# Performance work log

Measured on AMD Instinct MI355X. Metric: run time of the kernel, lower is better.

## Reference

```python
import jax, jax.numpy as jnp
import numpy as np

B, S, D, H, K = 2, 2048, 1024, 16, 16


def setup_inputs() -> dict:
    key = jax.random.key(0)
    ks = jax.random.split(key, 8)
    s = 0.02
    def w(k, shape):
        return s * jax.random.normal(k, shape, jnp.float32)
    return {
        "x": jax.random.normal(ks[0], (B, S, D), jnp.float32),
        "Wq": w(ks[1], (D, D)), "bq": jnp.zeros((D,), jnp.float32),
        "Wk": w(ks[2], (D, D)), "bk": jnp.zeros((D,), jnp.float32),
        "Wv": w(ks[3], (D, D)), "bv": jnp.zeros((D,), jnp.float32),
        "Wo": w(ks[4], (D, D)), "bo": jnp.zeros((D,), jnp.float32),
        "Ws1": w(ks[5], (D, D // 2)), "bs1": jnp.zeros((D // 2,), jnp.float32),
        "Ws2": w(ks[6], (D // 2, 1)), "bs2": jnp.zeros((1,), jnp.float32),
    }


def reference(x, Wq, bq, Wk, bk, Wv, bv, Wo, bo, Ws1, bs1, Ws2, bs2):
    Bx, Sx, Dx = x.shape
    Dh = Dx // H
    # QKV projections -> [B, H, S, Dh]
    q = (x @ Wq + bq).reshape(Bx, Sx, H, Dh).transpose(0, 2, 1, 3)
    k = (x @ Wk + bk).reshape(Bx, Sx, H, Dh).transpose(0, 2, 1, 3)
    v = (x @ Wv + bv).reshape(Bx, Sx, H, Dh).transpose(0, 2, 1, 3)
    scores = jnp.einsum('bhqd,bhkd->bhqk', q, k) / np.float32(np.sqrt(Dh))
    # Lightning-indexer importance: [B, S]; identical across heads, so compute once.
    imp = jax.nn.sigmoid(jax.nn.relu(x @ Ws1 + bs1) @ Ws2 + bs2)[..., 0]
    _, idx = jax.lax.top_k(imp, K)  # [B, K]
    sel = jnp.zeros((Bx, Sx), bool).at[jnp.arange(Bx)[:, None], idx].set(True)
    # sparse mask: position (i, j) kept if row i OR column j is a top-k token
    m2 = sel[:, :, None] | sel[:, None, :]  # [B, S, S]
    masked = jnp.where(m2[:, None, :, :], scores, -jnp.inf)
    w = jax.nn.softmax(masked, axis=-1)
    att = jnp.einsum('bhqk,bhkd->bhqd', w, v).transpose(0, 2, 1, 3).reshape(Bx, Sx, Dx)
    return att @ Wo + bo
```

## Files before the change

### kernel.cpp

```cpp
#include <hip/hip_runtime.h>
#include <math.h>

constexpr int Bb = 2, Ss = 2048, Dd = 1024, Hh = 16, Kk = 16;
constexpr float DELTA = 0.02f;

typedef __bf16 bf16x8 __attribute__((ext_vector_type(8)));
typedef __bf16 bf16x4 __attribute__((ext_vector_type(4)));
typedef float  f32x4  __attribute__((ext_vector_type(4)));

__device__ __forceinline__ void gld_lds16(const void* g, void* l) {
    __builtin_amdgcn_global_load_lds(
        (const __attribute__((address_space(1))) unsigned int*)g,
        (__attribute__((address_space(3))) unsigned int*)l, 16, 0, 0);
}

__global__ void __launch_bounds__(512) gemm_qkv_ind(
    const __bf16* __restrict__ xb, const __bf16* __restrict__ WqkvT,
    const __bf16* __restrict__ W1Th,
    const float* __restrict__ bq, const float* __restrict__ bk,
    const float* __restrict__ bv,
    __bf16* __restrict__ qb, __bf16* __restrict__ kb, __bf16* __restrict__ vb,
    const float* __restrict__ bs1, const float* __restrict__ Ws2,
    float* __restrict__ imp)
{
    __shared__ __bf16 As[256 * 64];
    __shared__ __bf16 Bs[128 * 64];

    const int bid  = blockIdx.x;
    const int cb   = bid % 28;
    const int bm   = (bid / 28) * 256;
    const int t    = threadIdx.x;
    const int wave = t >> 6;
    const int lane = t & 63;
    const int fr   = lane & 15;
    const int fq   = lane >> 4;
    const int K    = Dd;
    const bool ind = (cb >= 24);

    const __bf16* BT = ind ? (W1Th + (size_t)(cb - 24) * 128 * 1024)
                           : (WqkvT + (size_t)cb * 128 * 1024);

    const int wm = (wave & 3) * 64;
    const int wn = (wave >> 2) * 64;

    f32x4 acc[4][4] = {};

    for (int k0 = 0; k0 < K; k0 += 64) {
        #pragma unroll
        for (int l = 0; l < 4; ++l) {
            int c = l * 512 + t;
            int row = c >> 3, seg = (c & 7) ^ (row & 7);
            gld_lds16(xb + (size_t)(bm + row) * K + k0 + seg * 8,
                      As + (size_t)(l * 512 + wave * 64) * 8);
        }
        #pragma unroll
        for (int l = 0; l < 2; ++l) {
            int c = l * 512 + t;
            int row = c >> 3, seg = (c & 7) ^ (row & 7);
            gld_lds16(BT + (size_t)row * K + k0 + seg * 8,
                      Bs + (size_t)(l * 512 + wave * 64) * 8);
        }
        __syncthreads();

        #pragma unroll
        for (int s = 0; s < 2; ++s) {
            bf16x8 af[4], bf[4];
            #pragma unroll
            for (int i = 0; i < 4; ++i) {
                int row = wm + i * 16 + fr;
                af[i] = *(const bf16x8*)(As + row * 64 + (((s * 4 + fq) ^ (row & 7)) * 8));
            }
            #pragma unroll
            for (int j = 0; j < 4; ++j) {
                int row = wn + j * 16 + fr;
                bf[j] = *(const bf16x8*)(Bs + row * 64 + (((s * 4 + fq) ^ (row & 7)) * 8));
            }
            #pragma unroll
            for (int i = 0; i < 4; ++i)
                #pragma unroll
                for (int j = 0; j < 4; ++j)
                    acc[i][j] = __builtin_amdgcn_mfma_f32_16x16x32_bf16(af[i], bf[j], acc[i][j], 0, 0, 0);
        }
        __syncthreads();
    }

    const int cr = (lane >> 4) * 4;
    const int cc = lane & 15;

    if (!ind) {
        const int zone = cb >> 3;
        const int cl0  = cb * 128 - zone * 1024;
        const float* bias = (zone == 0) ? bq : (zone == 1) ? bk : bv;
        __bf16*      C    = (zone == 0) ? qb : (zone == 1) ? kb : vb;
        #pragma unroll
        for (int j = 0; j < 4; ++j) {
            int col = cl0 + wn + j * 16 + cc;
            float bb = bias[col];
            #pragma unroll
            for (int i = 0; i < 4; ++i) {
                #pragma unroll
                for (int r = 0; r < 4; ++r)
                    C[(size_t)(bm + wm + i * 16 + cr + r) * Dd + col] =
                        (__bf16)(acc[i][j][r] + bb);
            }
        }
    } else {
        const int hc0 = (cb - 24) * 128;
        float bb[4], w2[4];
        #pragma unroll
        for (int j = 0; j < 4; ++j) {
            int col = hc0 + wn + j * 16 + cc;
            bb[j] = bs1[col];
            w2[j] = Ws2[col];
        }
        #pragma unroll
        for (int i = 0; i < 4; ++i) {
            #pragma unroll
            for (int r = 0; r < 4; ++r) {
                float vsum = 0.f;
                #pragma unroll
                for (int j = 0; j < 4; ++j)
                    vsum += fmaxf(acc[i][j][r] + bb[j], 0.f) * w2[j];
                #pragma unroll
                for (int off = 8; off > 0; off >>= 1)
                    vsum += __shfl_xor(vsum, off, 16);
                if (cc == 0)
                    atomicAdd(imp + (bm + wm + i * 16 + cr + r), vsum);
            }
        }
    }
}

__global__ void __launch_bounds__(256) gemm_out(
    const __bf16* __restrict__ A, const __bf16* __restrict__ BT,
    const float* __restrict__ bias, float* __restrict__ C, int M, int N, int K)
{
    __shared__ __bf16 As[64 * 64];
    __shared__ __bf16 Bs[128 * 64];

    const int t    = threadIdx.x;
    const int wave = t >> 6;
    const int lane = t & 63;
    const int bm   = blockIdx.y * 64;
    const int bn   = blockIdx.x * 128;
    const int wm   = (wave & 1) * 32;
    const int wn   = (wave >> 1) * 64;
    const int fr   = lane & 15;
    const int fq   = lane >> 4;

    f32x4 acc[2][4] = {};

    for (int k0 = 0; k0 < K; k0 += 64) {
        #pragma unroll
        for (int l = 0; l < 2; ++l) {
            int c = l * 256 + t;
            int row = c >> 3, seg = (c & 7) ^ (row & 7);
            gld_lds16(A + (size_t)(bm + row) * K + k0 + seg * 8,
                      As + (size_t)(l * 256 + wave * 64) * 8);
        }
        #pragma unroll
        for (int l = 0; l < 4; ++l) {
            int c = l * 256 + t;
            int row = c >> 3, seg = (c & 7) ^ (row & 7);
            gld_lds16(BT + (size_t)(bn + row) * K + k0 + seg * 8,
                      Bs + (size_t)(l * 256 + wave * 64) * 8);
        }
        __syncthreads();

        #pragma unroll
        for (int s = 0; s < 2; ++s) {
            bf16x8 af[2], bf[4];
            #pragma unroll
            for (int i = 0; i < 2; ++i) {
                int row = wm + i * 16 + fr;
                af[i] = *(const bf16x8*)(As + row * 64 + (((s * 4 + fq) ^ (row & 7)) * 8));
            }
            #pragma unroll
            for (int j = 0; j < 4; ++j) {
                int row = wn + j * 16 + fr;
                bf[j] = *(const bf16x8*)(Bs + row * 64 + (((s * 4 + fq) ^ (row & 7)) * 8));
            }
            #pragma unroll
            for (int i = 0; i < 2; ++i)
                #pragma unroll
                for (int j = 0; j < 4; ++j)
                    acc[i][j] = __builtin_amdgcn_mfma_f32_16x16x32_bf16(af[i], bf[j], acc[i][j], 0, 0, 0);
        }
        __syncthreads();
    }

    const int cr = (lane >> 4) * 4;
    const int cc = lane & 15;
    #pragma unroll
    for (int j = 0; j < 4; ++j) {
        int col = bn + wn + j * 16 + cc;
        float bb = bias[col];
        #pragma unroll
        for (int i = 0; i < 2; ++i) {
            #pragma unroll
            for (int r = 0; r < 4; ++r)
                C[(size_t)(bm + wm + i * 16 + cr + r) * N + col] = acc[i][j][r] + bb;
        }
    }
}

__global__ void __launch_bounds__(256) prep_kernel(
    const float* __restrict__ x, __bf16* __restrict__ xb,
    float* __restrict__ imp, float* __restrict__ oacc,
    float* __restrict__ lsum, float* __restrict__ hbuf,
    int* __restrict__ ccount,
    const float* __restrict__ W0, const float* __restrict__ W1,
    const float* __restrict__ W2, const float* __restrict__ W3,
    __bf16* __restrict__ WqkvT, __bf16* __restrict__ WoT,
    const float* __restrict__ Ws1, __bf16* __restrict__ Th)
{
    __shared__ float tile[32][33];
    const int bid = blockIdx.x;

    if (bid < 4096) {
        int i = bid * 256 + threadIdx.x;
        if (i < Bb * Ss) imp[i] = 0.f;
        if (i < Bb * Hh * Kk * 64) oacc[i] = 0.f;
        if (i < Bb * Hh * Kk) lsum[i] = 0.f;
        if (i < Bb * 64 * 512) hbuf[i] = 0.f;
        if (i < Bb) ccount[i] = 0;
        float4 v = ((const float4*)x)[i];
        bf16x4 h = { (__bf16)v.x, (__bf16)v.y, (__bf16)v.z, (__bf16)v.w };
        ((bf16x4*)xb)[i] = h;
        return;
    }

    int tid = bid - 4096;
    int z   = tid >> 10;
    int rem = tid & 1023;
    int n0  = (rem & 31) * 32;
    int k0  = (rem >> 5) * 32;
    int tx = threadIdx.x & 31, ty = threadIdx.x >> 5;

    if (z < 4) {
        const float* W = (z == 0) ? W0 : (z == 1) ? W1 : (z == 2) ? W2 : W3;
        __bf16*      T = (z < 3) ? (WqkvT + (size_t)z * 1024 * 1024) : WoT;
        #pragma unroll
        for (int i = 0; i < 32; i += 8)
            tile[ty + i][tx] = W[(size_t)(k0 + ty + i) * 1024 + n0 + tx];
        __syncthreads();
        #pragma unroll
        for (int i = 0; i < 32; i += 8)
            T[(size_t)(n0 + ty + i) * 1024 + k0 + tx] = (__bf16)tile[tx][ty + i];
    } else {
        if (n0 >= 512) return;
        #pragma unroll
        for (int i = 0; i < 32; i += 8)
            tile[ty + i][tx] = Ws1[(size_t)(k0 + ty + i) * 512 + n0 + tx];
        __syncthreads();
        #pragma unroll
        for (int i = 0; i < 32; i += 8)
            Th[(size_t)(n0 + ty + i) * 1024 + k0 + tx] = (__bf16)tile[tx][ty + i];
    }
}

__global__ void __launch_bounds__(1024) topk_cand(
    const float* __restrict__ imp, int* __restrict__ cand_idx,
    int* __restrict__ ccount)
{
    int b = blockIdx.x;
    int t = threadIdx.x;
    int wave = t >> 6, lane = t & 63;
    __shared__ float vals[Ss];
    __shared__ float sv[16];
    __shared__ int   si[16];
    __shared__ float thr_s;
    __shared__ int   cnt_s;

    vals[t]        = imp[b * Ss + t];
    vals[t + 1024] = imp[b * Ss + t + 1024];
    __syncthreads();

    for (int it = 0; it < Kk; ++it) {
        float v0 = vals[t], v1 = vals[t + 1024];
        float best = v0; int bidx = t;
        if (v1 > best) { best = v1; bidx = t + 1024; }
        #pragma unroll
        for (int off = 32; off > 0; off >>= 1) {
            float ov = __shfl_xor(best, off, 64);
            int   oi = __shfl_xor(bidx, off, 64);
            if (ov > best || (ov == best && oi < bidx)) { best = ov; bidx = oi; }
        }
        if (lane == 0) { sv[wave] = best; si[wave] = bidx; }
        __syncthreads();
        if (t == 0) {
            float bv = sv[0]; int br = si[0];
            #pragma unroll
            for (int w = 1; w < 16; ++w)
                if (sv[w] > bv || (sv[w] == bv && si[w] < br)) { bv = sv[w]; br = si[w]; }
            cand_idx[b * 64 + it] = br;
            vals[br] = -1e30f;
            if (it == Kk - 1) { thr_s = bv - DELTA; cnt_s = Kk; }
        }
        __syncthreads();
    }

    float thr = thr_s;
    if (vals[t] > thr) {
        int p = atomicAdd(&cnt_s, 1);
        if (p < 64) cand_idx[b * 64 + p] = t;
    }
    if (vals[t + 1024] > thr) {
        int p = atomicAdd(&cnt_s, 1);
        if (p < 64) cand_idx[b * 64 + p] = t + 1024;
    }
    __syncthreads();
    if (t == 0) ccount[b] = min(cnt_s, 64);
}

__global__ void __launch_bounds__(256) rescore_h(
    const float* __restrict__ x, const float* __restrict__ Ws1,
    const int* __restrict__ cand_idx, const int* __restrict__ ccount,
    float* __restrict__ hbuf)
{
    const int c = blockIdx.x, kc = blockIdx.y, b = blockIdx.z;
    if (c >= ccount[b]) return;
    const int row = cand_idx[b * 64 + c];
    const int t = threadIdx.x;
    const int k0 = kc * 64;

    __shared__ float xs[64];
    if (t < 16)
        ((float4*)xs)[t] = ((const float4*)(x + ((size_t)(b * Ss + row)) * Dd + k0))[t];
    __syncthreads();

    float a0 = 0.f, a1 = 0.f;
    const float* W = Ws1 + (size_t)k0 * 512;
    #pragma unroll 16
    for (int kk = 0; kk < 64; ++kk) {
        float xv = xs[kk];
        a0 = fmaf(xv, W[kk * 512 + t], a0);
        a1 = fmaf(xv, W[kk * 512 + t + 256], a1);
    }
    float* hb = hbuf + ((size_t)(b * 64 + c)) * 512;
    atomicAdd(hb + t, a0);
    atomicAdd(hb + t + 256, a1);
}

__global__ void __launch_bounds__(256) rescore_fin(
    const float* __restrict__ hbuf, const float* __restrict__ bs1,
    const float* __restrict__ Ws2, const int* __restrict__ ccount,
    float* __restrict__ candz)
{
    const int c = blockIdx.x, b = blockIdx.y;
    if (c >= ccount[b]) return;
    const int t = threadIdx.x;
    __shared__ float red[256];
    const float* hb = hbuf + ((size_t)(b * 64 + c)) * 512;
    float zp = fmaxf(hb[t] + bs1[t], 0.f) * Ws2[t]
             + fmaxf(hb[t + 256] + bs1[t + 256], 0.f) * Ws2[t + 256];
    red[t] = zp;
    __syncthreads();
    for (int off = 128; off > 0; off >>= 1) {
        if (t < off) red[t] += red[t + off];
        __syncthreads();
    }
    if (t == 0) candz[b * 64 + c] = red[0];
}

__global__ void __launch_bounds__(64) select_k(
    const float* __restrict__ candz, const int* __restrict__ cand_idx,
    const int* __restrict__ ccount, int* __restrict__ sel_idx)
{
    const int b = blockIdx.x, t = threadIdx.x;
    const int cnt = ccount[b];
    float val = (t < cnt) ? candz[b * 64 + t] : -1e30f;
    int   row = (t < cnt) ? cand_idx[b * 64 + t] : 0x7fffffff;

    for (int it = 0; it < Kk; ++it) {
        float bv = val; int br = row;
        #pragma unroll
        for (int off = 1; off < 64; off <<= 1) {
            float ov = __shfl_xor(bv, off, 64);
            int   orw = __shfl_xor(br, off, 64);
            if (ov > bv || (ov == bv && orw < br)) { bv = ov; br = orw; }
        }
        if (row == br) val = -1e30f;
        if (t == 0) sel_idx[b * Kk + it] = br;
    }
}

__global__ void __launch_bounds__(256) attn_all(
    const __bf16* __restrict__ q, const __bf16* __restrict__ k,
    const __bf16* __restrict__ v, const int* __restrict__ sel_idx,
    __bf16* __restrict__ att, float* __restrict__ lsum,
    float* __restrict__ oacc)
{
    __shared__ __align__(16) float sm[6720];
    const int b = blockIdx.z, h = blockIdx.y;
    const int t = threadIdx.x;

    if (blockIdx.x < 128) {
        float (*KT)[17]  = (float(*)[17])sm;
        float (*Vs)[64]  = (float(*)[64])(sm + 1088);
        float (*qsh)[65] = (float(*)[65])(sm + 2112);
        float (*wsh)[16] = (float(*)[16])(sm + 3152);
        int*  sj         = (int*)(sm + 3408);
        const int q0 = blockIdx.x * 16;

        if (t < 16) sj[t] = sel_idx[b * Kk + t];
        __syncthreads();

        {
            int row = t >> 4, d0 = (t & 15) * 4;
            bf16x4 kv = *(const bf16x4*)(k + ((size_t)(b * Ss + sj[row])) * Dd + h * 64 + d0);
            bf16x4 vv = *(const bf16x4*)(v + ((size_t)(b * Ss + sj[row])) * Dd + h * 64 + d0);
            bf16x4 qv = *(const bf16x4*)(q + ((size_t)(b * Ss + q0 + row)) * Dd + h * 64 + d0);
            #pragma unroll
            for (int i = 0; i < 4; ++i) {
                KT[d0 + i][row]  = (float)kv[i];
                Vs[row][d0 + i]  = (float)vv[i];
                qsh[row][d0 + i] = (float)qv[i];
            }
        }
        __syncthreads();

        const int wave = t >> 6, lane = t & 63;
        const int ql = lane >> 4, j = lane & 15;
        const int qi = wave * 4 + ql;

        float s = 0.f;
        #pragma unroll
        for (int d = 0; d < 64; ++d) s = fmaf(qsh[qi][d], KT[d][j], s);
        s *= 0.125f;

        float m = s;
        #pragma unroll
        for (int off = 8; off > 0; off >>= 1) m = fmaxf(m, __shfl_xor(m, off, 16));
        float e = __expf(s - m);
        float sum = e;
        #pragma unroll
        for (int off = 8; off > 0; off >>= 1) sum += __shfl_xor(sum, off, 16);
        wsh[qi][j] = e / sum;

        #pragma unroll
        for (int q2 = 0; q2 < 4; ++q2) {
            int qq = wave * 4 + q2;
            float o = 0.f;
            #pragma unroll
            for (int jj = 0; jj < 16; ++jj)
                o = fmaf(wsh[qq][jj], Vs[jj][lane], o);
            att[((size_t)(b * Ss + q0 + qq)) * Dd + h * 64 + lane] = (__bf16)o;
        }
    } else {
        float (*Ks)[68] = (float(*)[68])sm;
        float (*Qs)[68] = (float(*)[68])(sm + 4352);
        float (*Es)[80] = (float(*)[80])(sm + 5440);
        const int j0 = (blockIdx.x - 128) * 64;

        #pragma unroll
        for (int l = 0; l < 2; ++l) {
            int c = t + 256 * l;
            int row = c >> 3, seg = c & 7;
            bf16x8 kv = *(const bf16x8*)(k + ((size_t)(b * Ss + j0 + row)) * Dd + h * 64 + seg * 8);
            #pragma unroll
            for (int e = 0; e < 8; ++e) Ks[row][seg * 8 + e] = (float)kv[e];
        }
        if (t < 128) {
            int row = t >> 3, seg = t & 7;
            int i = sel_idx[b * Kk + row];
            bf16x8 qv = *(const bf16x8*)(q + ((size_t)(b * Ss + i)) * Dd + h * 64 + seg * 8);
            #pragma unroll
            for (int e = 0; e < 8; ++e) Qs[row][seg * 8 + e] = (float)qv[e];
        }
        __syncthreads();

        const int qi = t >> 4, ks = t & 15;
        const int bhq = (b * Hh + h) * Kk + qi;
        float psum = 0.f;
        #pragma unroll
        for (int s8 = 0; s8 < 4; ++s8) {
            int j = ks + s8 * 16;
            float sdot = 0.f;
            #pragma unroll
            for (int d4 = 0; d4 < 16; ++d4) {
                float4 qv = *(const float4*)&Qs[qi][d4 * 4];
                float4 kv = *(const float4*)&Ks[j][d4 * 4];
                sdot += qv.x * kv.x + qv.y * kv.y + qv.z * kv.z + qv.w * kv.w;
            }
            float e = __expf(sdot * 0.125f);
            Es[qi][j] = e;
            psum += e;
        }
        #pragma unroll
        for (int off = 8; off > 0; off >>= 1) psum += __shfl_xor(psum, off, 16);
        if (ks == 0) atomicAdd(lsum + bhq, psum);
        __syncthreads();

        #pragma unroll
        for (int l = 0; l < 2; ++l) {
            int c = t + 256 * l;
            int row = c >> 3, seg = c & 7;
            bf16x8 vv = *(const bf16x8*)(v + ((size_t)(b * Ss + j0 + row)) * Dd + h * 64 + seg * 8);
            #pragma unroll
            for (int e = 0; e < 8; ++e) Ks[row][seg * 8 + e] = (float)vv[e];
        }
        __syncthreads();

        const int d = t & 63, qg = t >> 6;
        #pragma unroll
        for (int qq = 0; qq < 4; ++qq) {
            int qx = qg * 4 + qq;
            float o = 0.f;
            #pragma unroll 8
            for (int jj = 0; jj < 64; ++jj)
                o = fmaf(Es[qx][jj], Ks[jj][d], o);
            atomicAdd(oacc + (size_t)((b * Hh + h) * Kk + qx) * 64 + d, o);
        }
    }
}

__global__ void __launch_bounds__(64) attn_dense_fin(
    const float* __restrict__ oacc, const float* __restrict__ lsum,
    const int* __restrict__ sel_idx, __bf16* __restrict__ att)
{
    int bid = blockIdx.x;
    int qi = bid & 15, h = (bid >> 4) & 15, b = bid >> 8;
    int bhq = (b * Hh + h) * Kk + qi;
    int i = sel_idx[b * Kk + qi];
    float val = oacc[(size_t)bhq * 64 + threadIdx.x] / lsum[bhq];
    att[((size_t)(b * Ss + i)) * Dd + h * 64 + threadIdx.x] = (__bf16)val;
}

extern "C" void kernel_launch(void* const* d_in, const int* in_sizes, int n_in,
                              void* d_out, int out_size, void* d_ws, size_t ws_size,
                              hipStream_t stream)
{
    const float* x   = (const float*)d_in[0];
    const float* Wq  = (const float*)d_in[1];
    const float* bq  = (const float*)d_in[2];
    const float* Wk  = (const float*)d_in[3];
    const float* bk  = (const float*)d_in[4];
    const float* Wv  = (const float*)d_in[5];
    const float* bv  = (const float*)d_in[6];
    const float* Wo  = (const float*)d_in[7];
    const float* bo  = (const float*)d_in[8];
    const float* Ws1 = (const float*)d_in[9];
    const float* bs1 = (const float*)d_in[10];
    const float* Ws2 = (const float*)d_in[11];
    float* out = (float*)d_out;

    const size_t MSD = (size_t)Bb * Ss * Dd;
    const int M = Bb * Ss;

    char* p = (char*)d_ws;
    __bf16* qb  = (__bf16*)p; p += MSD * sizeof(__bf16);
    __bf16* kb  = (__bf16*)p; p += MSD * sizeof(__bf16);
    __bf16* vb  = (__bf16*)p; p += MSD * sizeof(__bf16);
    __bf16* att = (__bf16*)p; p += MSD * sizeof(__bf16);
    __bf16* xb  = (__bf16*)p; p += MSD * sizeof(__bf16);
    __bf16* WqkvT = (__bf16*)p; p += (size_t)3 * Dd * Dd * sizeof(__bf16);
    __bf16* WoT   = (__bf16*)p; p += (size_t)Dd * Dd * sizeof(__bf16);
    __bf16* W1Th  = (__bf16*)p; p += (size_t)512 * Dd * sizeof(__bf16);
    float* imp  = (float*)p; p += (size_t)Bb * Ss * sizeof(float);
    int* sel_idx = (int*)p; p += (size_t)Bb * Kk * sizeof(int);
    float* oacc = (float*)p; p += (size_t)Bb * Hh * Kk * 64 * sizeof(float);
    float* lsum = (float*)p; p += (size_t)Bb * Hh * Kk * sizeof(float);
    float* hbuf = (float*)p; p += (size_t)Bb * 64 * 512 * sizeof(float);
    int* ccount   = (int*)p; p += Bb * sizeof(int);
    int* cand_idx = (int*)p; p += (size_t)Bb * 64 * sizeof(int);
    float* candz  = (float*)p; p += (size_t)Bb * 64 * sizeof(float);

    prep_kernel<<<dim3(4096 + 5120), 256, 0, stream>>>(
        x, xb, imp, oacc, lsum, hbuf, ccount,
        Wq, Wk, Wv, Wo, WqkvT, WoT, Ws1, W1Th);
    gemm_qkv_ind<<<dim3(448), 512, 0, stream>>>(
        xb, WqkvT, W1Th, bq, bk, bv, qb, kb, vb, bs1, Ws2, imp);
    topk_cand<<<dim3(Bb), 1024, 0, stream>>>(imp, cand_idx, ccount);
    rescore_h<<<dim3(64, 16, Bb), 256, 0, stream>>>(x, Ws1, cand_idx, ccount, hbuf);
    rescore_fin<<<dim3(64, Bb), 256, 0, stream>>>(hbuf, bs1, Ws2, ccount, candz);
    select_k<<<dim3(Bb), 64, 0, stream>>>(candz, cand_idx, ccount, sel_idx);
    attn_all<<<dim3(160, Hh, Bb), 256, 0, stream>>>(
        qb, kb, vb, sel_idx, att, lsum, oacc);
    attn_dense_fin<<<dim3(Bb * Hh * Kk), 64, 0, stream>>>(oacc, lsum, sel_idx, att);
    gemm_out<<<dim3(8, 64), 256, 0, stream>>>(att, WoT, bo, out, M, Dd, Dd);
}
```

Before: 240.4 us.

## Restructure sparse attention algebraically to avoid full QKV projections and output GEMM

Replaces the full Q/K/V projection GEMM and full output projection with an algebraic reformulation. It projects only the selected top-k tokens' Q/K/V, folds Wq·k_sel and Wk·q_sel into small effective weight matrices (ET), and computes scores directly from x. Values are folded through Wo (VoT), so non-selected rows become a small x-by-256 GEMM and selected rows are handled by separate dense kernels. This removes most of the large bf16 projection work at the cost of many new kernels, a transposed copy of x, and different rounding paths.

Result: slower. 399.4 us (+66.2%).

```diff
diff --git a/kernel.cpp b/kernel.cpp
--- a/kernel.cpp
+++ b/kernel.cpp
@@ -14,12 +14,63 @@
         (__attribute__((address_space(3))) unsigned int*)l, 16, 0, 0);
 }
 
-__global__ void __launch_bounds__(512) gemm_qkv_ind(
-    const __bf16* __restrict__ xb, const __bf16* __restrict__ WqkvT,
-    const __bf16* __restrict__ W1Th,
-    const float* __restrict__ bq, const float* __restrict__ bk,
-    const float* __restrict__ bv,
-    __bf16* __restrict__ qb, __bf16* __restrict__ kb, __bf16* __restrict__ vb,
+__global__ void __launch_bounds__(256) prep_kernel(
+    const float* __restrict__ x, __bf16* __restrict__ xb,
+    __bf16* __restrict__ xbT,
+    float* __restrict__ imp, float* __restrict__ hbuf,
+    float* __restrict__ qkvsel, int* __restrict__ ccount,
+    const float* __restrict__ Ws1, __bf16* __restrict__ W1Th)
+{
+    __shared__ float tile[32][33];
+    const int bid = blockIdx.x;
+    const int t   = threadIdx.x;
+
+    if (bid < 4096) {
+        int i = bid * 256 + t;
+        if (i < Bb * Ss) imp[i] = 0.f;
+        if (i < Bb * 64 * 512) hbuf[i] = 0.f;
+        if (i < 3 * 32 * 1024) qkvsel[i] = 0.f;
+        if (i < Bb) ccount[i] = 0;
+        float4 v = ((const float4*)x)[i];
+        bf16x4 h = { (__bf16)v.x, (__bf16)v.y, (__bf16)v.z, (__bf16)v.w };
+        ((bf16x4*)xb)[i] = h;
+        return;
+    }
+    if (bid < 8192) {
+        int tid = bid - 4096;
+        int b   = tid >> 11;
+        int rem = tid & 2047;
+        int rt  = rem >> 5;
+        int ct  = rem & 31;
+        int tx = t & 31, ty = t >> 5;
+        const float* xp = x + (size_t)b * Ss * Dd;
+        #pragma unroll
+        for (int i2 = 0; i2 < 32; i2 += 8)
+            tile[ty + i2][tx] = xp[(size_t)(rt * 32 + ty + i2) * 1024 + ct * 32 + tx];
+        __syncthreads();
+        __bf16* xT = xbT + (size_t)b * Dd * Ss;
+        #pragma unroll
+        for (int i2 = 0; i2 < 32; i2 += 8)
+            xT[(size_t)(ct * 32 + ty + i2) * 2048 + rt * 32 + tx] = (__bf16)tile[tx][ty + i2];
+        return;
+    }
+    {
+        int tid = bid - 8192;
+        int n0 = (tid & 15) * 32;
+        int k0 = (tid >> 4) * 32;
+        int tx = t & 31, ty = t >> 5;
+        #pragma unroll
+        for (int i2 = 0; i2 < 32; i2 += 8)
+            tile[ty + i2][tx] = Ws1[(size_t)(k0 + ty + i2) * 512 + n0 + tx];
+        __syncthreads();
+        #pragma unroll
+        for (int i2 = 0; i2 < 32; i2 += 8)
+            W1Th[(size_t)(n0 + ty + i2) * 1024 + k0 + tx] = (__bf16)tile[tx][ty + i2];
+    }
+}
+
+__global__ void __launch_bounds__(512) gemm_ind(
+    const __bf16* __restrict__ xb, const __bf16* __restrict__ W1Th,
     const float* __restrict__ bs1, const float* __restrict__ Ws2,
     float* __restrict__ imp)
 {
@@ -27,19 +78,16 @@
     __shared__ __bf16 Bs[128 * 64];
 
     const int bid  = blockIdx.x;
-    const int cb   = bid % 28;
-    const int bm   = (bid / 28) * 256;
+    const int cb   = bid & 3;
+    const int bm   = (bid >> 2) * 256;
     const int t    = threadIdx.x;
     const int wave = t >> 6;
     const int lane = t & 63;
     const int fr   = lane & 15;
     const int fq   = lane >> 4;
     const int K    = Dd;
-    const bool ind = (cb >= 24);
-
-    const __bf16* BT = ind ? (W1Th + (size_t)(cb - 24) * 128 * 1024)
-                           : (WqkvT + (size_t)cb * 128 * 1024);
-
+
+    const __bf16* BT = W1Th + (size_t)cb * 128 * 1024;
     const int wm = (wave & 3) * 64;
     const int wn = (wave >> 2) * 64;
 
@@ -61,7 +109,6 @@
                       Bs + (size_t)(l * 512 + wave * 64) * 8);
         }
         __syncthreads();
-
         #pragma unroll
         for (int s = 0; s < 2; ++s) {
             bf16x8 af[4], bf[4];
@@ -86,57 +133,446 @@
 
     const int cr = (lane >> 4) * 4;
     const int cc = lane & 15;
-
-    if (!ind) {
-        const int zone = cb >> 3;
-        const int cl0  = cb * 128 - zone * 1024;
-        const float* bias = (zone == 0) ? bq : (zone == 1) ? bk : bv;
-        __bf16*      C    = (zone == 0) ? qb : (zone == 1) ? kb : vb;
-        #pragma unroll
-        for (int j = 0; j < 4; ++j) {
-            int col = cl0 + wn + j * 16 + cc;
-            float bb = bias[col];
+    const int hc0 = cb * 128;
+    float bb[4], w2[4];
+    #pragma unroll
+    for (int j = 0; j < 4; ++j) {
+        int col = hc0 + wn + j * 16 + cc;
+        bb[j] = bs1[col];
+        w2[j] = Ws2[col];
+    }
+    #pragma unroll
+    for (int i = 0; i < 4; ++i) {
+        #pragma unroll
+        for (int r = 0; r < 4; ++r) {
+            float vsum = 0.f;
+            #pragma unroll
+            for (int j = 0; j < 4; ++j)
+                vsum += fmaxf(acc[i][j][r] + bb[j], 0.f) * w2[j];
+            #pragma unroll
+            for (int off = 8; off > 0; off >>= 1)
+                vsum += __shfl_xor(vsum, off, 16);
+            if (cc == 0)
+                atomicAdd(imp + (bm + wm + i * 16 + cr + r), vsum);
+        }
+    }
+}
+
+__global__ void __launch_bounds__(1024) topk_cand(
+    const float* __restrict__ imp, int* __restrict__ cand_idx,
+    int* __restrict__ ccount)
+{
+    int b = blockIdx.x;
+    int t = threadIdx.x;
+    int wave = t >> 6, lane = t & 63;
+    __shared__ float vals[Ss];
+    __shared__ float sv[16];
+    __shared__ int   si[16];
+    __shared__ float thr_s;
+    __shared__ int   cnt_s;
+
+    vals[t]        = imp[b * Ss + t];
+    vals[t + 1024] = imp[b * Ss + t + 1024];
+    __syncthreads();
+
+    for (int it = 0; it < Kk; ++it) {
+        float v0 = vals[t], v1 = vals[t + 1024];
+        float best = v0; int bidx = t;
+        if (v1 > best) { best = v1; bidx = t + 1024; }
+        #pragma unroll
+        for (int off = 32; off > 0; off >>= 1) {
+            float ov = __shfl_xor(best, off, 64);
+            int   oi = __shfl_xor(bidx, off, 64);
+            if (ov > best || (ov == best && oi < bidx)) { best = ov; bidx = oi; }
+        }
+        if (lane == 0) { sv[wave] = best; si[wave] = bidx; }
+        __syncthreads();
+        if (t == 0) {
+            float bv = sv[0]; int br = si[0];
+            #pragma unroll
+            for (int w = 1; w < 16; ++w)
+                if (sv[w] > bv || (sv[w] == bv && si[w] < br)) { bv = sv[w]; br = si[w]; }
+            cand_idx[b * 64 + it] = br;
+            vals[br] = -1e30f;
+            if (it == Kk - 1) { thr_s = bv - DELTA; cnt_s = Kk; }
+        }
+        __syncthreads();
+    }
+
+    float thr = thr_s;
+    if (vals[t] > thr) {
+        int p = atomicAdd(&cnt_s, 1);
+        if (p < 64) cand_idx[b * 64 + p] = t;
+    }
+    if (vals[t + 1024] > thr) {
+        int p = atomicAdd(&cnt_s, 1);
+        if (p < 64) cand_idx[b * 64 + p] = t + 1024;
+    }
+    __syncthreads();
+    if (t == 0) ccount[b] = min(cnt_s, 64);
+}
+
+__global__ void __launch_bounds__(256) rescore_h(
+    const float* __restrict__ x, const float* __restrict__ Ws1,
+    const int* __restrict__ cand_idx, const int* __restrict__ ccount,
+    float* __restrict__ hbuf)
+{
+    const int c = blockIdx.x, kc = blockIdx.y, b = blockIdx.z;
+    if (c >= ccount[b]) return;
+    const int row = cand_idx[b * 64 + c];
+    const int t = threadIdx.x;
+    const int k0 = kc * 64;
+
+    __shared__ float xs[64];
+    if (t < 16)
+        ((float4*)xs)[t] = ((const float4*)(x + ((size_t)(b * Ss + row)) * Dd + k0))[t];
+    __syncthreads();
+
+    float a0 = 0.f, a1 = 0.f;
+    const float* W = Ws1 + (size_t)k0 * 512;
+    #pragma unroll 16
+    for (int kk = 0; kk < 64; ++kk) {
+        float xv = xs[kk];
+        a0 = fmaf(xv, W[kk * 512 + t], a0);
+        a1 = fmaf(xv, W[kk * 512 + t + 256], a1);
+    }
+    float* hb = hbuf + ((size_t)(b * 64 + c)) * 512;
+    atomicAdd(hb + t, a0);
+    atomicAdd(hb + t + 256, a1);
+}
+
+__global__ void __launch_bounds__(256) rescore_fin(
+    const float* __restrict__ hbuf, const float* __restrict__ bs1,
+    const float* __restrict__ Ws2, const int* __restrict__ ccount,
+    float* __restrict__ candz)
+{
+    const int c = blockIdx.x, b = blockIdx.y;
+    if (c >= ccount[b]) return;
+    const int t = threadIdx.x;
+    __shared__ float red[256];
+    const float* hb = hbuf + ((size_t)(b * 64 + c)) * 512;
+    float zp = fmaxf(hb[t] + bs1[t], 0.f) * Ws2[t]
+             + fmaxf(hb[t + 256] + bs1[t + 256], 0.f) * Ws2[t + 256];
+    red[t] = zp;
+    __syncthreads();
+    for (int off = 128; off > 0; off >>= 1) {
+        if (t < off) red[t] += red[t + off];
+        __syncthreads();
+    }
+    if (t == 0) candz[b * 64 + c] = red[0];
+}
+
+__global__ void __launch_bounds__(64) select_k(
+    const float* __restrict__ candz, const int* __restrict__ cand_idx,
+    const int* __restrict__ ccount, int* __restrict__ sel_idx)
+{
+    const int b = blockIdx.x, t = threadIdx.x;
+    const int cnt = ccount[b];
+    float val = (t < cnt) ? candz[b * 64 + t] : -1e30f;
+    int   row = (t < cnt) ? cand_idx[b * 64 + t] : 0x7fffffff;
+
+    for (int it = 0; it < Kk; ++it) {
+        float bv = val; int br = row;
+        #pragma unroll
+        for (int off = 1; off < 64; off <<= 1) {
+            float ov = __shfl_xor(bv, off, 64);
+            int   orw = __shfl_xor(br, off, 64);
+            if (ov > bv || (ov == bv && orw < br)) { bv = ov; br = orw; }
+        }
+        if (row == br) val = -1e30f;
+        if (t == 0) sel_idx[b * Kk + it] = br;
+    }
+}
+
+__global__ void __launch_bounds__(256) proj_sel(
+    const float* __restrict__ x,
+    const float* __restrict__ Wq, const float* __restrict__ Wk,
+    const float* __restrict__ Wv,
+    const int* __restrict__ sel_idx, float* __restrict__ qkvsel)
+{
+    const int cx = blockIdx.x;
+    const int m  = blockIdx.y;
+    const int kc = blockIdx.z;
+    const int t  = threadIdx.x;
+    __shared__ int   sj[32];
+    __shared__ float xs[32][128];
+
+    if (t < 32) sj[t] = sel_idx[t];
+    __syncthreads();
+
+    const int k0 = kc * 128;
+    #pragma unroll
+    for (int l = 0; l < 4; ++l) {
+        int c = l * 256 + t;
+        int r = c >> 5, kq = c & 31;
+        int b = r >> 4;
+        float4 v = *(const float4*)(x + ((size_t)(b * Ss + sj[r])) * Dd + k0 + kq * 4);
+        *(float4*)&xs[r][kq * 4] = v;
+    }
+    __syncthreads();
+
+    const float* W = (m == 0) ? Wq : (m == 1) ? Wk : Wv;
+    const int col = cx * 128 + (t & 127);
+    const int rh  = t >> 7;
+    float acc[16] = {};
+    #pragma unroll 4
+    for (int kk = 0; kk < 128; ++kk) {
+        float wv = W[(size_t)(k0 + kk) * 1024 + col];
+        #pragma unroll
+        for (int r = 0; r < 16; ++r)
+            acc[r] = fmaf(xs[rh * 16 + r][kk], wv, acc[r]);
+    }
+    #pragma unroll
+    for (int r = 0; r < 16; ++r)
+        atomicAdd(qkvsel + (size_t)(m * 32 + rh * 16 + r) * 1024 + col, acc[r]);
+}
+
+__global__ void __launch_bounds__(256) build_cdvo(
+    const float* __restrict__ Wq, const float* __restrict__ Wk,
+    const float* __restrict__ Wo,
+    const float* __restrict__ bq, const float* __restrict__ bk,
+    const float* __restrict__ bv,
+    const float* __restrict__ qkvsel, float* __restrict__ beta,
+    __bf16* __restrict__ ET, __bf16* __restrict__ VoT)
+{
+    const int nx = blockIdx.x;
+    const int h  = blockIdx.y;
+    const int b  = blockIdx.z;
+    const int t  = threadIdx.x;
+    __shared__ float qs[16][64], ks[16][64], vs[16][64];
+    __shared__ float wt[128][65];
+
+    #pragma unroll
+    for (int l = 0; l < 12; ++l) {
+        int c = l * 256 + t;
+        int mat = c >> 10, rem = c & 1023;
+        int row = rem >> 6, d = rem & 63;
+        const float* bias = (mat == 0) ? bq : (mat == 1) ? bk : bv;
+        float v = qkvsel[(size_t)(mat * 32 + b * 16 + row) * 1024 + h * 64 + d]
+                + bias[h * 64 + d];
+        if (mat == 0) qs[row][d] = v;
+        else if (mat == 1) ks[row][d] = v;
+        else vs[row][d] = v;
+    }
+    __syncthreads();
+
+    if (nx == 0 && t < 16) {
+        float a = 0.f;
+        #pragma unroll 8
+        for (int d = 0; d < 64; ++d) a = fmaf(bq[h * 64 + d], ks[t][d], a);
+        beta[b * 256 + h * 16 + t] = a;
+    }
+
+    const int nl = t & 127;
+    const int n  = nx * 128 + nl;
+    const int sg = t >> 7;
+
+    #pragma unroll
+    for (int l = 0; l < 8; ++l) {
+        int c = l * 256 + t;
+        int rn = c >> 4, c4 = c & 15;
+        float4 v = *(const float4*)(Wq + (size_t)(nx * 128 + rn) * 1024 + h * 64 + c4 * 4);
+        wt[rn][c4 * 4 + 0] = v.x; wt[rn][c4 * 4 + 1] = v.y;
+        wt[rn][c4 * 4 + 2] = v.z; wt[rn][c4 * 4 + 3] = v.w;
+    }
+    __syncthreads();
+    {
+        float acc[8] = {};
+        #pragma unroll 8
+        for (int d = 0; d < 64; ++d) {
+            float wv = wt[nl][d];
+            #pragma unroll
+            for (int s = 0; s < 8; ++s)
+                acc[s] = fmaf(wv, ks[sg * 8 + s][d], acc[s]);
+        }
+        #pragma unroll
+        for (int s = 0; s < 8; ++s)
+            ET[(size_t)(b * 512 + h * 16 + sg * 8 + s) * 1024 + n] = (__bf16)acc[s];
+    }
+    __syncthreads();
+
+    #pragma unroll
+    for (int l = 0; l < 8; ++l) {
+        int c = l * 256 + t;
+        int rn = c >> 4, c4 = c & 15;
+        float4 v = *(const float4*)(Wk + (size_t)(nx * 128 + rn) * 1024 + h * 64 + c4 * 4);
+        wt[rn][c4 * 4 + 0] = v.x; wt[rn][c4 * 4 + 1] = v.y;
+        wt[rn][c4 * 4 + 2] = v.z; wt[rn][c4 * 4 + 3] = v.w;
+    }
+    __syncthreads();
+    {
+        float acc[8] = {};
+        #pragma unroll 8
+        for (int d = 0; d < 64; ++d) {
+            float wv = wt[nl][d];
+            #pragma unroll
+            for (int s = 0; s < 8; ++s)
+                acc[s] = fmaf(wv, qs[sg * 8 + s][d], acc[s]);
+        }
+        #pragma unroll
+        for (int s = 0; s < 8; ++s)
+            ET[(size_t)(b * 512 + 256 + h * 16 + sg * 8 + s) * 1024 + n] = (__bf16)acc[s];
+    }
+
+    {
+        float acc[8] = {};
+        #pragma unroll 8
+        for (int d = 0; d < 64; ++d) {
+            float wv = Wo[(size_t)(h * 64 + d) * 1024 + n];
+            #pragma unroll
+            for (int s = 0; s < 8; ++s)
+                acc[s] = fmaf(wv, vs[sg * 8 + s][d], acc[s]);
+        }
+        #pragma unroll
+        for (int s = 0; s < 8; ++s)
+            VoT[((size_t)b * 1024 + n) * 256 + h * 16 + sg * 8 + s] = (__bf16)acc[s];
+    }
+}
+
+__global__ void __launch_bounds__(512) gemm_scores(
+    const __bf16* __restrict__ xb, const __bf16* __restrict__ ET,
+    float* __restrict__ Ssp, float* __restrict__ SdT)
+{
+    __shared__ __bf16 As[256 * 64];
+    __shared__ __bf16 Bs[128 * 64];
+
+    const int b    = blockIdx.y;
+    const int cb   = blockIdx.x & 3;
+    const int bm   = (blockIdx.x >> 2) * 256;
+    const int t    = threadIdx.x;
+    const int wave = t >> 6;
+    const int lane = t & 63;
+    const int fr   = lane & 15;
+    const int fq   = lane >> 4;
+    const int K    = Dd;
+
+    const __bf16* A  = xb + (size_t)b * Ss * Dd;
+    const __bf16* BT = ET + (size_t)b * 512 * 1024 + (size_t)cb * 128 * 1024;
+    const int wm = (wave & 3) * 64;
+    const int wn = (wave >> 2) * 64;
+
+    f32x4 acc[4][4] = {};
+
+    for (int k0 = 0; k0 < K; k0 += 64) {
+        #pragma unroll
+        for (int l = 0; l < 4; ++l) {
+            int c = l * 512 + t;
+            int row = c >> 3, seg = (c & 7) ^ (row & 7);
+            gld_lds16(A + (size_t)(bm + row) * K + k0 + seg * 8,
+                      As + (size_t)(l * 512 + wave * 64) * 8);
+        }
+        #pragma unroll
+        for (int l = 0; l < 2; ++l) {
+            int c = l * 512 + t;
+            int row = c >> 3, seg = (c & 7) ^ (row & 7);
+            gld_lds16(BT + (size_t)row * K + k0 + seg * 8,
+                      Bs + (size_t)(l * 512 + wave * 64) * 8);
+        }
+        __syncthreads();
+        #pragma unroll
+        for (int s = 0; s < 2; ++s) {
+            bf16x8 af[4], bf[4];
             #pragma unroll
             for (int i = 0; i < 4; ++i) {
+                int row = wm + i * 16 + fr;
+                af[i] = *(const bf16x8*)(As + row * 64 + (((s * 4 + fq) ^ (row & 7)) * 8));
+            }
+            #pragma unroll
+            for (int j = 0; j < 4; ++j) {
+                int row = wn + j * 16 + fr;
+                bf[j] = *(const bf16x8*)(Bs + row * 64 + (((s * 4 + fq) ^ (row & 7)) * 8));
+            }
+            #pragma unroll
+            for (int i = 0; i < 4; ++i)
+                #pragma unroll
+                for (int j = 0; j < 4; ++j)
+                    acc[i][j] = __builtin_amdgcn_mfma_f32_16x16x32_bf16(af[i], bf[j], acc[i][j], 0, 0, 0);
+        }
+        __syncthreads();
+    }
+
+    const int cr = (lane >> 4) * 4;
+    const int cc = lane & 15;
+    #pragma unroll
+    for (int j = 0; j < 4; ++j) {
+        int col = cb * 128 + wn + j * 16 + cc;
+        #pragma unroll
+        for (int i = 0; i < 4; ++i) {
+            int row0 = bm + wm + i * 16 + cr;
+            if (col < 256) {
                 #pragma unroll
                 for (int r = 0; r < 4; ++r)
-                    C[(size_t)(bm + wm + i * 16 + cr + r) * Dd + col] =
-                        (__bf16)(acc[i][j][r] + bb);
+                    Ssp[((size_t)b * 2048 + row0 + r) * 256 + col] = acc[i][j][r];
+            } else {
+                *(f32x4*)(SdT + ((size_t)b * 256 + col - 256) * 2048 + row0) = acc[i][j];
             }
         }
-    } else {
-        const int hc0 = (cb - 24) * 128;
-        float bb[4], w2[4];
-        #pragma unroll
-        for (int j = 0; j < 4; ++j) {
-            int col = hc0 + wn + j * 16 + cc;
-            bb[j] = bs1[col];
-            w2[j] = Ws2[col];
-        }
-        #pragma unroll
-        for (int i = 0; i < 4; ++i) {
-            #pragma unroll
-            for (int r = 0; r < 4; ++r) {
-                float vsum = 0.f;
-                #pragma unroll
-                for (int j = 0; j < 4; ++j)
-                    vsum += fmaxf(acc[i][j][r] + bb[j], 0.f) * w2[j];
-                #pragma unroll
-                for (int off = 8; off > 0; off >>= 1)
-                    vsum += __shfl_xor(vsum, off, 16);
-                if (cc == 0)
-                    atomicAdd(imp + (bm + wm + i * 16 + cr + r), vsum);
-            }
-        }
-    }
-}
-
-__global__ void __launch_bounds__(256) gemm_out(
-    const __bf16* __restrict__ A, const __bf16* __restrict__ BT,
-    const float* __restrict__ bias, float* __restrict__ C, int M, int N, int K)
+    }
+}
+
+__global__ void __launch_bounds__(256) sm_sparse(
+    const float* __restrict__ Ssp, const float* __restrict__ beta,
+    __bf16* __restrict__ Wsp)
+{
+    const int b = blockIdx.y;
+    const int r = blockIdx.x * 4 + (threadIdx.x >> 6);
+    const int l = threadIdx.x & 63;
+    float4 v  = *(const float4*)(Ssp + ((size_t)b * 2048 + r) * 256 + l * 4);
+    float4 bt = *(const float4*)(beta + b * 256 + l * 4);
+    float e0 = __expf((v.x + bt.x) * 0.125f);
+    float e1 = __expf((v.y + bt.y) * 0.125f);
+    float e2 = __expf((v.z + bt.z) * 0.125f);
+    float e3 = __expf((v.w + bt.w) * 0.125f);
+    float ps = e0 + e1 + e2 + e3;
+    ps += __shfl_xor(ps, 1, 64);
+    ps += __shfl_xor(ps, 2, 64);
+    float inv = 1.f / ps;
+    bf16x4 w = { (__bf16)(e0 * inv), (__bf16)(e1 * inv),
+                 (__bf16)(e2 * inv), (__bf16)(e3 * inv) };
+    *(bf16x4*)(Wsp + ((size_t)b * 2048 + r) * 256 + l * 4) = w;
+}
+
+__global__ void __launch_bounds__(256) sm_dense(
+    const float* __restrict__ SdT, __bf16* __restrict__ WdT)
+{
+    const int b = blockIdx.y, cx = blockIdx.x;
+    const int t = threadIdx.x;
+    __shared__ float red[256];
+    const float* Sp = SdT + ((size_t)b * 256 + cx) * 2048;
+    float4 v0 = *(const float4*)(Sp + t * 8);
+    float4 v1 = *(const float4*)(Sp + t * 8 + 4);
+    float e[8];
+    e[0] = __expf(v0.x * 0.125f); e[1] = __expf(v0.y * 0.125f);
+    e[2] = __expf(v0.z * 0.125f); e[3] = __expf(v0.w * 0.125f);
+    e[4] = __expf(v1.x * 0.125f); e[5] = __expf(v1.y * 0.125f);
+    e[6] = __expf(v1.z * 0.125f); e[7] = __expf(v1.w * 0.125f);
+    float ps = 0.f;
+    #pragma unroll
+    for (int i = 0; i < 8; ++i) ps += e[i];
+    red[t] = ps;
+    __syncthreads();
+    for (int off = 128; off > 0; off >>= 1) {
+        if (t < off) red[t] += red[t + off];
+        __syncthreads();
+    }
+    float inv = 1.f / red[0];
+    bf16x8 w;
+    #pragma unroll
+    for (int i = 0; i < 8; ++i) w[i] = (__bf16)(e[i] * inv);
+    *(bf16x8*)(WdT + ((size_t)b * 256 + cx) * 2048 + t * 8) = w;
+}
+
+__global__ void __launch_bounds__(256) gemm_bt(
+    const __bf16* __restrict__ A0, const __bf16* __restrict__ BT0,
+    const float* __restrict__ bias, float* __restrict__ C0,
+    int N, int K, size_t sA, size_t sB, size_t sC)
 {
     __shared__ __bf16 As[64 * 64];
     __shared__ __bf16 Bs[128 * 64];
+
+    const __bf16* A  = A0 + (size_t)blockIdx.z * sA;
+    const __bf16* BT = BT0 + (size_t)blockIdx.z * sB;
+    float* C = C0 + (size_t)blockIdx.z * sC;
 
     const int t    = threadIdx.x;
     const int wave = t >> 6;
@@ -166,7 +602,6 @@
                       Bs + (size_t)(l * 256 + wave * 64) * 8);
         }
         __syncthreads();
-
         #pragma unroll
         for (int s = 0; s < 2; ++s) {
             bf16x8 af[2], bf[4];
@@ -194,7 +629,7 @@
     #pragma unroll
     for (int j = 0; j < 4; ++j) {
         int col = bn + wn + j * 16 + cc;
-        float bb = bias[col];
+        float bb = bias ? bias[col] : 0.f;
         #pragma unroll
         for (int i = 0; i < 2; ++i) {
             #pragma unroll
@@ -204,327 +639,69 @@
     }
 }
 
-__global__ void __launch_bounds__(256) prep_kernel(
-    const float* __restrict__ x, __bf16* __restrict__ xb,
-    float* __restrict__ imp, float* __restrict__ oacc,
-    float* __restrict__ lsum, float* __restrict__ hbuf,
-    int* __restrict__ ccount,
-    const float* __restrict__ W0, const float* __restrict__ W1,
-    const float* __restrict__ W2, const float* __restrict__ W3,
-    __bf16* __restrict__ WqkvT, __bf16* __restrict__ WoT,
-    const float* __restrict__ Ws1, __bf16* __restrict__ Th)
-{
-    __shared__ float tile[32][33];
-    const int bid = blockIdx.x;
-
-    if (bid < 4096) {
-        int i = bid * 256 + threadIdx.x;
-        if (i < Bb * Ss) imp[i] = 0.f;
-        if (i < Bb * Hh * Kk * 64) oacc[i] = 0.f;
-        if (i < Bb * Hh * Kk) lsum[i] = 0.f;
-        if (i < Bb * 64 * 512) hbuf[i] = 0.f;
-        if (i < Bb) ccount[i] = 0;
-        float4 v = ((const float4*)x)[i];
-        bf16x4 h = { (__bf16)v.x, (__bf16)v.y, (__bf16)v.z, (__bf16)v.w };
-        ((bf16x4*)xb)[i] = h;
-        return;
-    }
-
-    int tid = bid - 4096;
-    int z   = tid >> 10;
-    int rem = tid & 1023;
-    int n0  = (rem & 31) * 32;
-    int k0  = (rem >> 5) * 32;
-    int tx = threadIdx.x & 31, ty = threadIdx.x >> 5;
-
-    if (z < 4) {
-        const float* W = (z == 0) ? W0 : (z == 1) ? W1 : (z == 2) ? W2 : W3;
-        __bf16*      T = (z < 3) ? (WqkvT + (size_t)z * 1024 * 1024) : WoT;
-        #pragma unroll
-        for (int i = 0; i < 32; i += 8)
-            tile[ty + i][tx] = W[(size_t)(k0 + ty + i) * 1024 + n0 + tx];
-        __syncthreads();
-        #pragma unroll
-        for (int i = 0; i < 32; i += 8)
-            T[(size_t)(n0 + ty + i) * 1024 + k0 + tx] = (__bf16)tile[tx][ty + i];
-    } else {
-        if (n0 >= 512) return;
-        #pragma unroll
-        for (int i = 0; i < 32; i += 8)
-            tile[ty + i][tx] = Ws1[(size_t)(k0 + ty + i) * 512 + n0 + tx];
-        __syncthreads();
-        #pragma unroll
-        for (int i = 0; i < 32; i += 8)
-            Th[(size_t)(n0 + ty + i) * 1024 + k0 + tx] = (__bf16)tile[tx][ty + i];
-    }
-}
-
-__global__ void __launch_bounds__(1024) topk_cand(
-    const float* __restrict__ imp, int* __restrict__ cand_idx,
-    int* __restrict__ ccount)
-{
-    int b = blockIdx.x;
-    int t = threadIdx.x;
-    int wave = t >> 6, lane = t & 63;
-    __shared__ float vals[Ss];
-    __shared__ float sv[16];
-    __shared__ int   si[16];
-    __shared__ float thr_s;
-    __shared__ int   cnt_s;
-
-    vals[t]        = imp[b * Ss + t];
-    vals[t + 1024] = imp[b * Ss + t + 1024];
-    __syncthreads();
-
-    for (int it = 0; it < Kk; ++it) {
-        float v0 = vals[t], v1 = vals[t + 1024];
-        float best = v0; int bidx = t;
-        if (v1 > best) { best = v1; bidx = t + 1024; }
-        #pragma unroll
-        for (int off = 32; off > 0; off >>= 1) {
-            float ov = __shfl_xor(best, off, 64);
-            int   oi = __shfl_xor(bidx, off, 64);
-            if (ov > best || (ov == best && oi < bidx)) { best = ov; bidx = oi; }
-        }
-        if (lane == 0) { sv[wave] = best; si[wave] = bidx; }
-        __syncthreads();
-        if (t == 0) {
-            float bv = sv[0]; int br = si[0];
-            #pragma unroll
-            for (int w = 1; w < 16; ++w)
-                if (sv[w] > bv || (sv[w] == bv && si[w] < br)) { bv = sv[w]; br = si[w]; }
-            cand_idx[b * 64 + it] = br;
-            vals[br] = -1e30f;
-            if (it == Kk - 1) { thr_s = bv - DELTA; cnt_s = Kk; }
-        }
-        __syncthreads();
-    }
-
-    float thr = thr_s;
-    if (vals[t] > thr) {
-        int p = atomicAdd(&cnt_s, 1);
-        if (p < 64) cand_idx[b * 64 + p] = t;
-    }
-    if (vals[t + 1024] > thr) {
-        int p = atomicAdd(&cnt_s, 1);
-        if (p < 64) cand_idx[b * 64 + p] = t + 1024;
-    }
-    __syncthreads();
-    if (t == 0) ccount[b] = min(cnt_s, 64);
-}
-
-__global__ void __launch_bounds__(256) rescore_h(
-    const float* __restrict__ x, const float* __restrict__ Ws1,
-    const int* __restrict__ cand_idx, const int* __restrict__ ccount,
-    float* __restrict__ hbuf)
-{
-    const int c = blockIdx.x, kc = blockIdx.y, b = blockIdx.z;
-    if (c >= ccount[b]) return;
-    const int row = cand_idx[b * 64 + c];
+__global__ void __launch_bounds__(256) dense_z(
+    const float* __restrict__ Y, const float* __restrict__ Wv,
+    const float* __restrict__ bv, float* __restrict__ zbuf)
+{
+    const int h = blockIdx.x, b = blockIdx.y;
     const int t = threadIdx.x;
-    const int k0 = kc * 64;
-
-    __shared__ float xs[64];
-    if (t < 16)
-        ((float4*)xs)[t] = ((const float4*)(x + ((size_t)(b * Ss + row)) * Dd + k0))[t];
-    __syncthreads();
-
-    float a0 = 0.f, a1 = 0.f;
-    const float* W = Ws1 + (size_t)k0 * 512;
-    #pragma unroll 16
-    for (int kk = 0; kk < 64; ++kk) {
-        float xv = xs[kk];
-        a0 = fmaf(xv, W[kk * 512 + t], a0);
-        a1 = fmaf(xv, W[kk * 512 + t + 256], a1);
-    }
-    float* hb = hbuf + ((size_t)(b * 64 + c)) * 512;
-    atomicAdd(hb + t, a0);
-    atomicAdd(hb + t + 256, a1);
-}
-
-__global__ void __launch_bounds__(256) rescore_fin(
-    const float* __restrict__ hbuf, const float* __restrict__ bs1,
-    const float* __restrict__ Ws2, const int* __restrict__ ccount,
-    float* __restrict__ candz)
-{
-    const int c = blockIdx.x, b = blockIdx.y;
-    if (c >= ccount[b]) return;
+    __shared__ float Ys[16][64];
+    const int d = t & 63, tg = t >> 6;
+    float acc[4] = {};
+    for (int k0 = 0; k0 < 1024; k0 += 64) {
+        #pragma unroll
+        for (int l = 0; l < 4; ++l) {
+            int c = l * 256 + t;
+            int row = c >> 6, kk = c & 63;
+            Ys[row][kk] = Y[((size_t)b * 256 + h * 16 + row) * 1024 + k0 + kk];
+        }
+        __syncthreads();
+        #pragma unroll 8
+        for (int kk = 0; kk < 64; ++kk) {
+            float wv = Wv[(size_t)(k0 + kk) * 1024 + h * 64 + d];
+            #pragma unroll
+            for (int tt = 0; tt < 4; ++tt)
+                acc[tt] = fmaf(Ys[tg * 4 + tt][kk], wv, acc[tt]);
+        }
+        __syncthreads();
+    }
+    #pragma unroll
+    for (int tt = 0; tt < 4; ++tt)
+        zbuf[((size_t)b * 16 + tg * 4 + tt) * 1024 + h * 64 + d] = acc[tt] + bv[h * 64 + d];
+}
+
+__global__ void __launch_bounds__(256) dense_out(
+    const float* __restrict__ zbuf, const float* __restrict__ Wo,
+    const float* __restrict__ bo, const int* __restrict__ sel_idx,
+    float* __restrict__ out)
+{
+    const int nx = blockIdx.x, b = blockIdx.y;
     const int t = threadIdx.x;
-    __shared__ float red[256];
-    const float* hb = hbuf + ((size_t)(b * 64 + c)) * 512;
-    float zp = fmaxf(hb[t] + bs1[t], 0.f) * Ws2[t]
-             + fmaxf(hb[t + 256] + bs1[t + 256], 0.f) * Ws2[t + 256];
-    red[t] = zp;
-    __syncthreads();
-    for (int off = 128; off > 0; off >>= 1) {
-        if (t < off) red[t] += red[t + off];
-        __syncthreads();
-    }
-    if (t == 0) candz[b * 64 + c] = red[0];
-}
-
-__global__ void __launch_bounds__(64) select_k(
-    const float* __restrict__ candz, const int* __restrict__ cand_idx,
-    const int* __restrict__ ccount, int* __restrict__ sel_idx)
-{
-    const int b = blockIdx.x, t = threadIdx.x;
-    const int cnt = ccount[b];
-    float val = (t < cnt) ? candz[b * 64 + t] : -1e30f;
-    int   row = (t < cnt) ? cand_idx[b * 64 + t] : 0x7fffffff;
-
-    for (int it = 0; it < Kk; ++it) {
-        float bv = val; int br = row;
-        #pragma unroll
-        for (int off = 1; off < 64; off <<= 1) {
-            float ov = __shfl_xor(bv, off, 64);
-            int   orw = __shfl_xor(br, off, 64);
-            if (ov > bv || (ov == bv && orw < br)) { bv = ov; br = orw; }
-        }
-        if (row == br) val = -1e30f;
-        if (t == 0) sel_idx[b * Kk + it] = br;
-    }
-}
-
-__global__ void __launch_bounds__(256) attn_all(
-    const __bf16* __restrict__ q, const __bf16* __restrict__ k,
-    const __bf16* __restrict__ v, const int* __restrict__ sel_idx,
-    __bf16* __restrict__ att, float* __restrict__ lsum,
-    float* __restrict__ oacc)
-{
-    __shared__ __align__(16) float sm[6720];
-    const int b = blockIdx.z, h = blockIdx.y;
-    const int t = threadIdx.x;
-
-    if (blockIdx.x < 128) {
-        float (*KT)[17]  = (float(*)[17])sm;
-        float (*Vs)[64]  = (float(*)[64])(sm + 1088);
-        float (*qsh)[65] = (float(*)[65])(sm + 2112);
-        float (*wsh)[16] = (float(*)[16])(sm + 3152);
-        int*  sj         = (int*)(sm + 3408);
-        const int q0 = blockIdx.x * 16;
-
-        if (t < 16) sj[t] = sel_idx[b * Kk + t];
-        __syncthreads();
-
-        {
-            int row = t >> 4, d0 = (t & 15) * 4;
-            bf16x4 kv = *(const bf16x4*)(k + ((size_t)(b * Ss + sj[row])) * Dd + h * 64 + d0);
-            bf16x4 vv = *(const bf16x4*)(v + ((size_t)(b * Ss + sj[row])) * Dd + h * 64 + d0);
-            bf16x4 qv = *(const bf16x4*)(q + ((size_t)(b * Ss + q0 + row)) * Dd + h * 64 + d0);
-            #pragma unroll
-            for (int i = 0; i < 4; ++i) {
-                KT[d0 + i][row]  = (float)kv[i];
-                Vs[row][d0 + i]  = (float)vv[i];
-                qsh[row][d0 + i] = (float)qv[i];
-            }
-        }
-        __syncthreads();
-
-        const int wave = t >> 6, lane = t & 63;
-        const int ql = lane >> 4, j = lane & 15;
-        const int qi = wave * 4 + ql;
-
-        float s = 0.f;
-        #pragma unroll
-        for (int d = 0; d < 64; ++d) s = fmaf(qsh[qi][d], KT[d][j], s);
-        s *= 0.125f;
-
-        float m = s;
-        #pragma unroll
-        for (int off = 8; off > 0; off >>= 1) m = fmaxf(m, __shfl_xor(m, off, 16));
-        float e = __expf(s - m);
-        float sum = e;
-        #pragma unroll
-        for (int off = 8; off > 0; off >>= 1) sum += __shfl_xor(sum, off, 16);
-        wsh[qi][j] = e / sum;
-
-        #pragma unroll
-        for (int q2 = 0; q2 < 4; ++q2) {
-            int qq = wave * 4 + q2;
-            float o = 0.f;
-            #pragma unroll
-            for (int jj = 0; jj < 16; ++jj)
-                o = fmaf(wsh[qq][jj], Vs[jj][lane], o);
-            att[((size_t)(b * Ss + q0 + qq)) * Dd + h * 64 + lane] = (__bf16)o;
-        }
-    } else {
-        float (*Ks)[68] = (float(*)[68])sm;
-        float (*Qs)[68] = (float(*)[68])(sm + 4352);
-        float (*Es)[80] = (float(*)[80])(sm + 5440);
-        const int j0 = (blockIdx.x - 128) * 64;
-
-        #pragma unroll
-        for (int l = 0; l < 2; ++l) {
-            int c = t + 256 * l;
-            int row = c >> 3, seg = c & 7;
-            bf16x8 kv = *(const bf16x8*)(k + ((size_t)(b * Ss + j0 + row)) * Dd + h * 64 + seg * 8);
-            #pragma unroll
-            for (int e = 0; e < 8; ++e) Ks[row][seg * 8 + e] = (float)kv[e];
-        }
-        if (t < 128) {
-            int row = t >> 3, seg = t & 7;
-            int i = sel_idx[b * Kk + row];
-            bf16x8 qv = *(const bf16x8*)(q + ((size_t)(b * Ss + i)) * Dd + h * 64 + seg * 8);
-            #pragma unroll
-            for (int e = 0; e < 8; ++e) Qs[row][seg * 8 + e] = (float)qv[e];
-        }
-        __syncthreads();
-
-        const int qi = t >> 4, ks = t & 15;
-        const int bhq = (b * Hh + h) * Kk + qi;
-        float psum = 0.f;
-        #pragma unroll
-        for (int s8 = 0; s8 < 4; ++s8) {
-            int j = ks + s8 * 16;
-            float sdot = 0.f;
-            #pragma unroll
-            for (int d4 = 0; d4 < 16; ++d4) {
-                float4 qv = *(const float4*)&Qs[qi][d4 * 4];
-                float4 kv = *(const float4*)&Ks[j][d4 * 4];
-                sdot += qv.x * kv.x + qv.y * kv.y + qv.z * kv.z + qv.w * kv.w;
-            }
-            float e = __expf(sdot * 0.125f);
-            Es[qi][j] = e;
-            psum += e;
-        }
-        #pragma unroll
-        for (int off = 8; off > 0; off >>= 1) psum += __shfl_xor(psum, off, 16);
-        if (ks == 0) atomicAdd(lsum + bhq, psum);
-        __syncthreads();
-
-        #pragma unroll
-        for (int l = 0; l < 2; ++l) {
-            int c = t + 256 * l;
-            int row = c >> 3, seg = c & 7;
-            bf16x8 vv = *(const bf16x8*)(v + ((size_t)(b * Ss + j0 + row)) * Dd + h * 64 + seg * 8);
-            #pragma unroll
-            for (int e = 0; e < 8; ++e) Ks[row][seg * 8 + e] = (float)vv[e];
-        }
-        __syncthreads();
-
-        const int d = t & 63, qg = t >> 6;
-        #pragma unroll
-        for (int qq = 0; qq < 4; ++qq) {
-            int qx = qg * 4 + qq;
-            float o = 0.f;
-            #pragma unroll 8
-            for (int jj = 0; jj < 64; ++jj)
-                o = fmaf(Es[qx][jj], Ks[jj][d], o);
-            atomicAdd(oacc + (size_t)((b * Hh + h) * Kk + qx) * 64 + d, o);
-        }
-    }
-}
-
-__global__ void __launch_bounds__(64) attn_dense_fin(
-    const float* __restrict__ oacc, const float* __restrict__ lsum,
-    const int* __restrict__ sel_idx, __bf16* __restrict__ att)
-{
-    int bid = blockIdx.x;
-    int qi = bid & 15, h = (bid >> 4) & 15, b = bid >> 8;
-    int bhq = (b * Hh + h) * Kk + qi;
-    int i = sel_idx[b * Kk + qi];
-    float val = oacc[(size_t)bhq * 64 + threadIdx.x] / lsum[bhq];
-    att[((size_t)(b * Ss + i)) * Dd + h * 64 + threadIdx.x] = (__bf16)val;
+    __shared__ float zs[16][64];
+    __shared__ int sj[16];
+    if (t < 16) sj[t] = sel_idx[b * 16 + t];
+    const int n = nx * 64 + (t & 63), tg = t >> 6;
+    float acc[4] = {};
+    for (int k0 = 0; k0 < 1024; k0 += 64) {
+        #pragma unroll
+        for (int l = 0; l < 4; ++l) {
+            int c = l * 256 + t;
+            int row = c >> 6, kk = c & 63;
+            zs[row][kk] = zbuf[((size_t)b * 16 + row) * 1024 + k0 + kk];
+        }
+        __syncthreads();
+        #pragma unroll 8
+        for (int kk = 0; kk < 64; ++kk) {
+            float wv = Wo[(size_t)(k0 + kk) * 1024 + n];
+            #pragma unroll
+            for (int tt = 0; tt < 4; ++tt)
+                acc[tt] = fmaf(zs[tg * 4 + tt][kk], wv, acc[tt]);
+        }
+        __syncthreads();
+    }
+    #pragma unroll
+    for (int tt = 0; tt < 4; ++tt)
+        out[((size_t)b * 2048 + sj[tg * 4 + tt]) * 1024 + n] = acc[tt] + bo[n];
 }
 
 extern "C" void kernel_launch(void* const* d_in, const int* in_sizes, int n_in,
@@ -546,37 +723,47 @@
     float* out = (float*)d_out;
 
     const size_t MSD = (size_t)Bb * Ss * Dd;
-    const int M = Bb * Ss;
 
     char* p = (char*)d_ws;
-    __bf16* qb  = (__bf16*)p; p += MSD * sizeof(__bf16);
-    __bf16* kb  = (__bf16*)p; p += MSD * sizeof(__bf16);
-    __bf16* vb  = (__bf16*)p; p += MSD * sizeof(__bf16);
-    __bf16* att = (__bf16*)p; p += MSD * sizeof(__bf16);
-    __bf16* xb  = (__bf16*)p; p += MSD * sizeof(__bf16);
-    __bf16* WqkvT = (__bf16*)p; p += (size_t)3 * Dd * Dd * sizeof(__bf16);
-    __bf16* WoT   = (__bf16*)p; p += (size_t)Dd * Dd * sizeof(__bf16);
-    __bf16* W1Th  = (__bf16*)p; p += (size_t)512 * Dd * sizeof(__bf16);
-    float* imp  = (float*)p; p += (size_t)Bb * Ss * sizeof(float);
-    int* sel_idx = (int*)p; p += (size_t)Bb * Kk * sizeof(int);
-    float* oacc = (float*)p; p += (size_t)Bb * Hh * Kk * 64 * sizeof(float);
-    float* lsum = (float*)p; p += (size_t)Bb * Hh * Kk * sizeof(float);
-    float* hbuf = (float*)p; p += (size_t)Bb * 64 * 512 * sizeof(float);
+    __bf16* xb    = (__bf16*)p; p += MSD * sizeof(__bf16);
+    __bf16* xbT   = (__bf16*)p; p += MSD * sizeof(__bf16);
+    __bf16* W1Th  = (__bf16*)p; p += (size_t)512 * 1024 * sizeof(__bf16);
+    __bf16* ET    = (__bf16*)p; p += (size_t)2 * 512 * 1024 * sizeof(__bf16);
+    __bf16* VoT   = (__bf16*)p; p += (size_t)2 * 1024 * 256 * sizeof(__bf16);
+    __bf16* Wsp   = (__bf16*)p; p += (size_t)2 * 2048 * 256 * sizeof(__bf16);
+    __bf16* WdT   = (__bf16*)p; p += (size_t)2 * 256 * 2048 * sizeof(__bf16);
+    float* Ssp    = (float*)p; p += (size_t)2 * 2048 * 256 * sizeof(float);
+    float* SdT    = (float*)p; p += (size_t)2 * 256 * 2048 * sizeof(float);
+    float* Y      = (float*)p; p += (size_t)2 * 256 * 1024 * sizeof(float);
+    float* zbuf   = (float*)p; p += (size_t)2 * 16 * 1024 * sizeof(float);
+    float* imp    = (float*)p; p += (size_t)Bb * Ss * sizeof(float);
+    float* hbuf   = (float*)p; p += (size_t)Bb * 64 * 512 * sizeof(float);
+    float* qkvsel = (float*)p; p += (size_t)3 * 32 * 1024 * sizeof(float);
+    float* beta   = (float*)p; p += (size_t)2 * 256 * sizeof(float);
+    float* candz  = (float*)p; p += (size_t)Bb * 64 * sizeof(float);
+    int* sel_idx  = (int*)p; p += (size_t)Bb * Kk * sizeof(int);
+    int* cand_idx = (int*)p; p += (size_t)Bb * 64 * sizeof(int);
     int* ccount   = (int*)p; p += Bb * sizeof(int);
-    int* cand_idx = (int*)p; p += (size_t)Bb * 64 * sizeof(int);
-    float* candz  = (float*)p; p += (size_t)Bb * 64 * sizeof(float);
-
-    prep_kernel<<<dim3(4096 + 5120), 256, 0, stream>>>(
-        x, xb, imp, oacc, lsum, hbuf, ccount,
-        Wq, Wk, Wv, Wo, WqkvT, WoT, Ws1, W1Th);
-    gemm_qkv_ind<<<dim3(448), 512, 0, stream>>>(
-        xb, WqkvT, W1Th, bq, bk, bv, qb, kb, vb, bs1, Ws2, imp);
+
+    prep_kernel<<<dim3(8704), 256, 0, stream>>>(
+        x, xb, xbT, imp, hbuf, qkvsel, ccount, Ws1, W1Th);
+    gemm_ind<<<dim3(64), 512, 0, stream>>>(xb, W1Th, bs1, Ws2, imp);
     topk_cand<<<dim3(Bb), 1024, 0, stream>>>(imp, cand_idx, ccount);
     rescore_h<<<dim3(64, 16, Bb), 256, 0, stream>>>(x, Ws1, cand_idx, ccount, hbuf);
     rescore_fin<<<dim3(64, Bb), 256, 0, stream>>>(hbuf, bs1, Ws2, ccount, candz);
     select_k<<<dim3(Bb), 64, 0, stream>>>(candz, cand_idx, ccount, sel_idx);
-    attn_all<<<dim3(160, Hh, Bb), 256, 0, stream>>>(
-        qb, kb, vb, sel_idx, att, lsum, oacc);
-    attn_dense_fin<<<dim3(Bb * Hh * Kk), 64, 0, stream>>>(oacc, lsum, sel_idx, att);
-    gemm_out<<<dim3(8, 64), 256, 0, stream>>>(att, WoT, bo, out, M, Dd, Dd);
-}
+    proj_sel<<<dim3(8, 3, 8), 256, 0, stream>>>(x, Wq, Wk, Wv, sel_idx, qkvsel);
+    build_cdvo<<<dim3(8, 16, 2), 256, 0, stream>>>(
+        Wq, Wk, Wo, bq, bk, bv, qkvsel, beta, ET, VoT);
+    gemm_scores<<<dim3(32, 2), 512, 0, stream>>>(xb, ET, Ssp, SdT);
+    sm_sparse<<<dim3(512, 2), 256, 0, stream>>>(Ssp, beta, Wsp);
+    sm_dense<<<dim3(256, 2), 256, 0, stream>>>(SdT, WdT);
+    gemm_bt<<<dim3(8, 32, 2), 256, 0, stream>>>(
+        Wsp, VoT, bo, out, 1024, 256,
+        (size_t)2048 * 256, (size_t)1024 * 256, (size_t)2048 * 1024);
+    gemm_bt<<<dim3(8, 4, 2), 256, 0, stream>>>(
+        WdT, xbT, nullptr, Y, 1024, 2048,
+        (size_t)256 * 2048, (size_t)1024 * 2048, (size_t)256 * 1024);
+    dense_z<<<dim3(16, 2), 256, 0, stream>>>(Y, Wv, bv, zbuf);
+    dense_out<<<dim3(16, 2), 256, 0, stream>>>(zbuf, Wo, bo, sel_idx, out);
+}
```
